# Kernel optimization log

Measured on AMD Instinct MI355X. Metric: run time of the kernel, lower is better.

## Reference

```python
import jax, jax.numpy as jnp
import numpy as np

N = 8192
D = 64  # node feature width
E = 64  # edge-derived feature width


def setup_inputs() -> dict:
    key = jax.random.key(0)
    k1, k2, k3 = jax.random.split(key, 3)
    # Dense normalized adjacency (module stores normalize(A).toarray()); values in [0,1).
    A = jax.random.uniform(k1, (N, N), dtype=jnp.float32) / N  # scaled like a normalized adjacency
    F = jax.random.normal(k2, (N, D), dtype=jnp.float32)
    new_features = jax.random.normal(k3, (N, E), dtype=jnp.float32)
    return {"A": A, "F": F, "new_features": new_features}


def reference(A, F, new_features):
    # layer 1: node branch gets ReLU, edge-feature branch does not
    h = jax.nn.relu(A @ F)              # [N, D]
    g = A @ new_features                # [N, E]
    # layer 2
    h = jax.nn.relu(A @ h)              # [N, D]
    g = A @ g                           # [N, E]
    return jnp.concatenate([h, g], axis=-1)  # [N, D+E]
```

## Files before the change

### kernel.cpp

```cpp
#include <hip/hip_runtime.h>
#include <hip/hip_bf16.h>


typedef unsigned short ushort_t;
typedef __attribute__((ext_vector_type(8))) short short8;
typedef __attribute__((ext_vector_type(4))) float f32x4;
typedef __attribute__((ext_vector_type(4))) unsigned short us4;

#define NN 8192
#define NO 128
#define BKK 64
#define KSPAN 2048
#define GITERS (KSPAN / BKK)

__global__ void detect_dtype(const ushort_t* __restrict__ A, int* __restrict__ flag) {
  __shared__ int smax, szero;
  const int t = threadIdx.x;
  if (t == 0) { smax = 0; szero = 0; }
  __syncthreads();
  int lmax = 0, lzero = 0;
  #pragma unroll
  for (int j = 0; j < 8; ++j) {
    int idx = t * 8 + j;
    int u = (int)A[idx];
    if ((idx & 1) == 0) {
      lmax = max(lmax, u);
      lzero += (u == 0) ? 1 : 0;
    }
  }
  atomicMax(&smax, lmax);
  atomicAdd(&szero, lzero);
  __syncthreads();
  if (t == 0) *flag = (smax > 0x3A00 || szero > 800) ? 1 : 0;
}

__global__ void zero_ws(float* __restrict__ p) {
  size_t i = ((size_t)blockIdx.x * 256 + threadIdx.x) * 4;
  *(float4*)(p + i) = make_float4(0.f, 0.f, 0.f, 0.f);
}

__device__ __forceinline__ short bf16bits(float x) {
  __hip_bfloat16 h = __float2bfloat16(x);
  return *reinterpret_cast<short*>(&h);
}

__device__ __forceinline__ short8 cvt8(float4 a, float4 b) {
  short8 r;
  r[0] = bf16bits(a.x); r[1] = bf16bits(a.y); r[2] = bf16bits(a.z); r[3] = bf16bits(a.w);
  r[4] = bf16bits(b.x); r[5] = bf16bits(b.y); r[6] = bf16bits(b.z); r[7] = bf16bits(b.w);
  return r;
}

__global__ void pack_bt(const ushort_t* __restrict__ F, const ushort_t* __restrict__ NF,
                        ushort_t* __restrict__ Bt, const int* __restrict__ flag) {
  int idx = blockIdx.x * 256 + threadIdx.x;
  int n = idx >> 10;
  int k0 = (idx & 1023) << 3;
  ushort_t* dst = Bt + ((size_t)n << 13) + k0;
  if (*flag) {
    const float* src = (n < 64) ? ((const float*)F + n) : ((const float*)NF + (n - 64));
    #pragma unroll
    for (int j = 0; j < 8; ++j) dst[j] = (ushort_t)bf16bits(src[(size_t)(k0 + j) << 6]);
  } else {
    const ushort_t* src = (n < 64) ? (F + n) : (NF + (n - 64));
    #pragma unroll
    for (int j = 0; j < 8; ++j) dst[j] = src[(size_t)(k0 + j) << 6];
  }
}

__device__ __forceinline__ void compute_tile(const ushort_t* bA, const ushort_t* bB,
                                             int w, int lane, f32x4 (&acc)[4][2]) {
  #pragma unroll
  for (int s = 0; s < 2; ++s) {
    short8 b0 = *(const short8*)(bB + (4 * w + s) * 512 + lane * 8);
    short8 b1 = *(const short8*)(bB + (4 * w + 2 + s) * 512 + lane * 8);
    #pragma unroll
    for (int mt = 0; mt < 4; ++mt) {
      short8 a = *(const short8*)(bA + (2 * mt + s) * 512 + lane * 8);
      acc[mt][0] = __builtin_amdgcn_mfma_f32_16x16x32_bf16(a, b0, acc[mt][0], 0, 0, 0);
      acc[mt][1] = __builtin_amdgcn_mfma_f32_16x16x32_bf16(a, b1, acc[mt][1], 0, 0, 0);
    }
  }
}

__global__ __launch_bounds__(256) void gemm_atomic(
    const ushort_t* __restrict__ Au, const float* __restrict__ Af,
    const ushort_t* __restrict__ Bt, float* __restrict__ P,
    const int* __restrict__ flag) {
  __shared__ __align__(16) ushort_t lsA[2][8 * 512];
  __shared__ __align__(16) ushort_t lsB[2][16 * 512];
  const int t = threadIdx.x;
  const int w = t >> 6, lane = t & 63;
  const int mtile = blockIdx.x >> 2;
  const int split = blockIdx.x & 3;
  const size_t m0 = (size_t)mtile * 64;
  const int kb = split * KSPAN;

  const int wh = w >> 1, ws_ = w & 1;
  const int l15 = lane & 15, lq = lane >> 4;
  const size_t rowA0 = m0 + (size_t)wh * 16 + l15;
  const size_t colb = (size_t)kb + ws_ * 32 + lq * 8;
  const ushort_t* gA0b = Au + rowA0 * NN + colb;
  const ushort_t* gA1b = gA0b + (size_t)32 * NN;
  const float*    gA0f = Af + rowA0 * NN + colb;
  const float*    gA1f = gA0f + (size_t)32 * NN;
  const ushort_t* gB0 = Bt + ((size_t)wh * 16 + l15) * NN + colb;

  const f32x4 zero = {0.f, 0.f, 0.f, 0.f};
  f32x4 acc[4][2];
  #pragma unroll
  for (int mt = 0; mt < 4; ++mt) { acc[mt][0] = zero; acc[mt][1] = zero; }

  const int fl = *flag;

  if (fl) {
    float4 a00 = *(const float4*)gA0f;
    float4 a01 = *(const float4*)(gA0f + 4);
    float4 a10 = *(const float4*)gA1f;
    float4 a11 = *(const float4*)(gA1f + 4);
    short8 rb0 = *(const short8*)gB0;
    short8 rb1 = *(const short8*)(gB0 + (size_t)32 * NN);
    short8 rb2 = *(const short8*)(gB0 + (size_t)64 * NN);
    short8 rb3 = *(const short8*)(gB0 + (size_t)96 * NN);
    gA0f += BKK; gA1f += BKK; gB0 += BKK;
    *(short8*)(lsA[0] + t * 8) = cvt8(a00, a01);
    *(short8*)(lsA[0] + t * 8 + 2048) = cvt8(a10, a11);
    *(short8*)(lsB[0] + t * 8) = rb0;
    *(short8*)(lsB[0] + t * 8 + 2048) = rb1;
    *(short8*)(lsB[0] + t * 8 + 4096) = rb2;
    *(short8*)(lsB[0] + t * 8 + 6144) = rb3;
    __syncthreads();
    int buf = 0;
    for (int it = 0; it < GITERS - 1; ++it) {
      a00 = *(const float4*)gA0f;
      a01 = *(const float4*)(gA0f + 4);
      a10 = *(const float4*)gA1f;
      a11 = *(const float4*)(gA1f + 4);
      rb0 = *(const short8*)gB0;
      rb1 = *(const short8*)(gB0 + (size_t)32 * NN);
      rb2 = *(const short8*)(gB0 + (size_t)64 * NN);
      rb3 = *(const short8*)(gB0 + (size_t)96 * NN);
      gA0f += BKK; gA1f += BKK; gB0 += BKK;
      compute_tile(lsA[buf], lsB[buf], w, lane, acc);
      const int nb = buf ^ 1;
      *(short8*)(lsA[nb] + t * 8) = cvt8(a00, a01);
      *(short8*)(lsA[nb] + t * 8 + 2048) = cvt8(a10, a11);
      *(short8*)(lsB[nb] + t * 8) = rb0;
      *(short8*)(lsB[nb] + t * 8 + 2048) = rb1;
      *(short8*)(lsB[nb] + t * 8 + 4096) = rb2;
      *(short8*)(lsB[nb] + t * 8 + 6144) = rb3;
      __syncthreads();
      buf = nb;
    }
    compute_tile(lsA[buf], lsB[buf], w, lane, acc);
  } else {
    short8 ra0 = *(const short8*)gA0b;
    short8 ra1 = *(const short8*)gA1b;
    short8 rb0 = *(const short8*)gB0;
    short8 rb1 = *(const short8*)(gB0 + (size_t)32 * NN);
    short8 rb2 = *(const short8*)(gB0 + (size_t)64 * NN);
    short8 rb3 = *(const short8*)(gB0 + (size_t)96 * NN);
    gA0b += BKK; gA1b += BKK; gB0 += BKK;
    *(short8*)(lsA[0] + t * 8) = ra0;
    *(short8*)(lsA[0] + t * 8 + 2048) = ra1;
    *(short8*)(lsB[0] + t * 8) = rb0;
    *(short8*)(lsB[0] + t * 8 + 2048) = rb1;
    *(short8*)(lsB[0] + t * 8 + 4096) = rb2;
    *(short8*)(lsB[0] + t * 8 + 6144) = rb3;
    __syncthreads();
    int buf = 0;
    for (int it = 0; it < GITERS - 1; ++it) {
      ra0 = *(const short8*)gA0b;
      ra1 = *(const short8*)gA1b;
      rb0 = *(const short8*)gB0;
      rb1 = *(const short8*)(gB0 + (size_t)32 * NN);
      rb2 = *(const short8*)(gB0 + (size_t)64 * NN);
      rb3 = *(const short8*)(gB0 + (size_t)96 * NN);
      gA0b += BKK; gA1b += BKK; gB0 += BKK;
      compute_tile(lsA[buf], lsB[buf], w, lane, acc);
      const int nb = buf ^ 1;
      *(short8*)(lsA[nb] + t * 8) = ra0;
      *(short8*)(lsA[nb] + t * 8 + 2048) = ra1;
      *(short8*)(lsB[nb] + t * 8) = rb0;
      *(short8*)(lsB[nb] + t * 8 + 2048) = rb1;
      *(short8*)(lsB[nb] + t * 8 + 4096) = rb2;
      *(short8*)(lsB[nb] + t * 8 + 6144) = rb3;
      __syncthreads();
      buf = nb;
    }
    compute_tile(lsA[buf], lsB[buf], w, lane, acc);
  }

  const int cn0 = 32 * w + l15;
  const int rb = lq * 4;
  #pragma unroll
  for (int mt = 0; mt < 4; ++mt) {
    float* dst = P + (m0 + mt * 16 + rb) * NO;
    #pragma unroll
    for (int reg = 0; reg < 4; ++reg) {
      unsafeAtomicAdd(&dst[(size_t)reg * NO + cn0], acc[mt][0][reg]);
      unsafeAtomicAdd(&dst[(size_t)reg * NO + cn0 + 16], acc[mt][1][reg]);
    }
  }
}

__global__ void epi_t(const float* __restrict__ P, ushort_t* __restrict__ Ct) {
  __shared__ ushort_t lt[128 * 65];
  const size_t base = (size_t)blockIdx.x * (64 * NO);
  const int t = threadIdx.x;
  for (int i = 0; i < 32; ++i) {
    int e = i * 256 + t;
    int n = e & 127, m = e >> 7;
    float v = P[base + e];
    if (n < 64) v = fmaxf(v, 0.f);
    lt[n * 65 + m] = (ushort_t)bf16bits(v);
  }
  __syncthreads();
  const int n = t >> 1, h = t & 1;
  const size_t m0 = (size_t)blockIdx.x * 64;
  ushort_t* dst = Ct + (size_t)n * NN + m0 + h * 32;
  #pragma unroll
  for (int j = 0; j < 32; ++j) dst[j] = lt[n * 65 + h * 32 + j];
}

__global__ void epi_out(const float* __restrict__ P, ushort_t* __restrict__ outb,
                        float* __restrict__ outf, const int* __restrict__ flag) {
  int idx = blockIdx.x * 256 + threadIdx.x;
  size_t e = (size_t)idx * 4;
  float4 v = *(const float4*)(P + e);
  float s[4] = {v.x, v.y, v.z, v.w};
  int n0 = (int)(e & 127);
  #pragma unroll
  for (int j = 0; j < 4; ++j) if (n0 + j < 64) s[j] = fmaxf(s[j], 0.f);
  if (*flag) {
    *(float4*)(outf + e) = make_float4(s[0], s[1], s[2], s[3]);
  } else {
    us4 r;
    #pragma unroll
    for (int j = 0; j < 4; ++j) r[j] = (ushort_t)bf16bits(s[j]);
    *(us4*)(outb + e) = r;
  }
}

extern "C" void kernel_launch(void* const* d_in, const int* in_sizes, int n_in,
                              void* d_out, int out_size, void* d_ws, size_t ws_size,
                              hipStream_t stream) {
  const ushort_t* A  = (const ushort_t*)d_in[0];
  const ushort_t* F  = (const ushort_t*)d_in[1];
  const ushort_t* NF = (const ushort_t*)d_in[2];

  char* ws = (char*)d_ws;
  ushort_t* Bt = (ushort_t*)(ws);
  ushort_t* Ct = (ushort_t*)(ws + (2u << 20));
  float*    P1 = (float*)(ws + (4u << 20));
  float*    P2 = (float*)(ws + (8u << 20));
  int*    flag = (int*)(ws + (12u << 20));

  detect_dtype<<<1, 256, 0, stream>>>(A, flag);
  zero_ws<<<2048, 256, 0, stream>>>(P1);
  pack_bt<<<512, 256, 0, stream>>>(F, NF, Bt, flag);
  gemm_atomic<<<512, 256, 0, stream>>>(A, (const float*)A, Bt, P1, flag);
  epi_t<<<128, 256, 0, stream>>>(P1, Ct);
  gemm_atomic<<<512, 256, 0, stream>>>(A, (const float*)A, Ct, P2, flag);
  epi_out<<<1024, 256, 0, stream>>>(P2, (ushort_t*)d_out, (float*)d_out, flag);
}
```

Before: 483.7 us.

## Cache bf16 copy of A in first GEMM, use direct global-to-LDS loads, split K by eight

On the fp32 input path, the first GEMM converts A to bf16 and also writes that copy to workspace, so the second GEMM can read half the bytes using global_load_lds direct copies. Split-K grows from 4 to 8, doubling the grid, and double buffering is replaced by single-buffered LDS with two barriers per iteration. The epi_t store loop is vectorised to 16-byte writes. This adds a 128MB workspace write in the first GEMM and drops prefetch overlap in exchange for reduced traffic in the second GEMM.

```diff
diff --git a/kernel.cpp b/kernel.cpp
--- a/kernel.cpp
+++ b/kernel.cpp
@@ -10,7 +10,8 @@
 #define NN 8192
 #define NO 128
 #define BKK 64
-#define KSPAN 2048
+#define NSPLIT 8
+#define KSPAN (NN / NSPLIT)
 #define GITERS (KSPAN / BKK)
 
 __global__ void detect_dtype(const ushort_t* __restrict__ A, int* __restrict__ flag) {
@@ -49,6 +50,12 @@
   r[0] = bf16bits(a.x); r[1] = bf16bits(a.y); r[2] = bf16bits(a.z); r[3] = bf16bits(a.w);
   r[4] = bf16bits(b.x); r[5] = bf16bits(b.y); r[6] = bf16bits(b.z); r[7] = bf16bits(b.w);
   return r;
+}
+
+__device__ __forceinline__ void gl2lds16(const ushort_t* g, ushort_t* l) {
+  __builtin_amdgcn_global_load_lds(
+      (const __attribute__((address_space(1))) void*)g,
+      (__attribute__((address_space(3))) void*)l, 16, 0, 0);
 }
 
 __global__ void pack_bt(const ushort_t* __restrict__ F, const ushort_t* __restrict__ NF,
@@ -85,14 +92,14 @@
 
 __global__ __launch_bounds__(256) void gemm_atomic(
     const ushort_t* __restrict__ Au, const float* __restrict__ Af,
-    const ushort_t* __restrict__ Bt, float* __restrict__ P,
-    const int* __restrict__ flag) {
-  __shared__ __align__(16) ushort_t lsA[2][8 * 512];
-  __shared__ __align__(16) ushort_t lsB[2][16 * 512];
+    ushort_t* __restrict__ Abf, const ushort_t* __restrict__ Bt,
+    float* __restrict__ P, const int* __restrict__ flag, int wb, int rdabf) {
+  __shared__ __align__(16) ushort_t lsA[8 * 512];
+  __shared__ __align__(16) ushort_t lsB[16 * 512];
   const int t = threadIdx.x;
   const int w = t >> 6, lane = t & 63;
-  const int mtile = blockIdx.x >> 2;
-  const int split = blockIdx.x & 3;
+  const int mtile = blockIdx.x >> 3;
+  const int split = blockIdx.x & 7;
   const size_t m0 = (size_t)mtile * 64;
   const int kb = split * KSPAN;
 
@@ -100,10 +107,8 @@
   const int l15 = lane & 15, lq = lane >> 4;
   const size_t rowA0 = m0 + (size_t)wh * 16 + l15;
   const size_t colb = (size_t)kb + ws_ * 32 + lq * 8;
-  const ushort_t* gA0b = Au + rowA0 * NN + colb;
-  const ushort_t* gA1b = gA0b + (size_t)32 * NN;
-  const float*    gA0f = Af + rowA0 * NN + colb;
-  const float*    gA1f = gA0f + (size_t)32 * NN;
+  const size_t offA0 = rowA0 * NN + colb;
+  const size_t offA1 = offA0 + (size_t)32 * NN;
   const ushort_t* gB0 = Bt + ((size_t)wh * 16 + l15) * NN + colb;
 
   const f32x4 zero = {0.f, 0.f, 0.f, 0.f};
@@ -113,82 +118,56 @@
 
   const int fl = *flag;
 
-  if (fl) {
-    float4 a00 = *(const float4*)gA0f;
-    float4 a01 = *(const float4*)(gA0f + 4);
-    float4 a10 = *(const float4*)gA1f;
-    float4 a11 = *(const float4*)(gA1f + 4);
-    short8 rb0 = *(const short8*)gB0;
-    short8 rb1 = *(const short8*)(gB0 + (size_t)32 * NN);
-    short8 rb2 = *(const short8*)(gB0 + (size_t)64 * NN);
-    short8 rb3 = *(const short8*)(gB0 + (size_t)96 * NN);
-    gA0f += BKK; gA1f += BKK; gB0 += BKK;
-    *(short8*)(lsA[0] + t * 8) = cvt8(a00, a01);
-    *(short8*)(lsA[0] + t * 8 + 2048) = cvt8(a10, a11);
-    *(short8*)(lsB[0] + t * 8) = rb0;
-    *(short8*)(lsB[0] + t * 8 + 2048) = rb1;
-    *(short8*)(lsB[0] + t * 8 + 4096) = rb2;
-    *(short8*)(lsB[0] + t * 8 + 6144) = rb3;
-    __syncthreads();
-    int buf = 0;
-    for (int it = 0; it < GITERS - 1; ++it) {
-      a00 = *(const float4*)gA0f;
-      a01 = *(const float4*)(gA0f + 4);
-      a10 = *(const float4*)gA1f;
-      a11 = *(const float4*)(gA1f + 4);
-      rb0 = *(const short8*)gB0;
-      rb1 = *(const short8*)(gB0 + (size_t)32 * NN);
-      rb2 = *(const short8*)(gB0 + (size_t)64 * NN);
-      rb3 = *(const short8*)(gB0 + (size_t)96 * NN);
+  if (fl && !rdabf) {
+    const float* gA0f = Af + offA0;
+    const float* gA1f = Af + offA1;
+    ushort_t* pW0 = Abf + offA0;
+    ushort_t* pW1 = Abf + offA1;
+    for (int it = 0; it < GITERS; ++it) {
+      float4 a00 = *(const float4*)gA0f;
+      float4 a01 = *(const float4*)(gA0f + 4);
+      float4 a10 = *(const float4*)gA1f;
+      float4 a11 = *(const float4*)(gA1f + 4);
+      short8 rb0 = *(const short8*)gB0;
+      short8 rb1 = *(const short8*)(gB0 + (size_t)32 * NN);
+      short8 rb2 = *(const short8*)(gB0 + (size_t)64 * NN);
+      short8 rb3 = *(const short8*)(gB0 + (size_t)96 * NN);
       gA0f += BKK; gA1f += BKK; gB0 += BKK;
-      compute_tile(lsA[buf], lsB[buf], w, lane, acc);
-      const int nb = buf ^ 1;
-      *(short8*)(lsA[nb] + t * 8) = cvt8(a00, a01);
-      *(short8*)(lsA[nb] + t * 8 + 2048) = cvt8(a10, a11);
-      *(short8*)(lsB[nb] + t * 8) = rb0;
-      *(short8*)(lsB[nb] + t * 8 + 2048) = rb1;
-      *(short8*)(lsB[nb] + t * 8 + 4096) = rb2;
-      *(short8*)(lsB[nb] + t * 8 + 6144) = rb3;
-      __syncthreads();
-      buf = nb;
-    }
-    compute_tile(lsA[buf], lsB[buf], w, lane, acc);
+      short8 c0 = cvt8(a00, a01);
+      short8 c1 = cvt8(a10, a11);
+      if (wb) {
+        *(short8*)pW0 = c0;
+        *(short8*)pW1 = c1;
+        pW0 += BKK; pW1 += BKK;
+      }
+      *(short8*)(lsA + t * 8) = c0;
+      *(short8*)(lsA + t * 8 + 2048) = c1;
+      *(short8*)(lsB + t * 8) = rb0;
+      *(short8*)(lsB + t * 8 + 2048) = rb1;
+      *(short8*)(lsB + t * 8 + 4096) = rb2;
+      *(short8*)(lsB + t * 8 + 6144) = rb3;
+      __syncthreads();
+      compute_tile(lsA, lsB, w, lane, acc);
+      __syncthreads();
+    }
   } else {
-    short8 ra0 = *(const short8*)gA0b;
-    short8 ra1 = *(const short8*)gA1b;
-    short8 rb0 = *(const short8*)gB0;
-    short8 rb1 = *(const short8*)(gB0 + (size_t)32 * NN);
-    short8 rb2 = *(const short8*)(gB0 + (size_t)64 * NN);
-    short8 rb3 = *(const short8*)(gB0 + (size_t)96 * NN);
-    gA0b += BKK; gA1b += BKK; gB0 += BKK;
-    *(short8*)(lsA[0] + t * 8) = ra0;
-    *(short8*)(lsA[0] + t * 8 + 2048) = ra1;
-    *(short8*)(lsB[0] + t * 8) = rb0;
-    *(short8*)(lsB[0] + t * 8 + 2048) = rb1;
-    *(short8*)(lsB[0] + t * 8 + 4096) = rb2;
-    *(short8*)(lsB[0] + t * 8 + 6144) = rb3;
-    __syncthreads();
-    int buf = 0;
-    for (int it = 0; it < GITERS - 1; ++it) {
-      ra0 = *(const short8*)gA0b;
-      ra1 = *(const short8*)gA1b;
-      rb0 = *(const short8*)gB0;
-      rb1 = *(const short8*)(gB0 + (size_t)32 * NN);
-      rb2 = *(const short8*)(gB0 + (size_t)64 * NN);
-      rb3 = *(const short8*)(gB0 + (size_t)96 * NN);
-      gA0b += BKK; gA1b += BKK; gB0 += BKK;
-      compute_tile(lsA[buf], lsB[buf], w, lane, acc);
-      const int nb = buf ^ 1;
-      *(short8*)(lsA[nb] + t * 8) = ra0;
-      *(short8*)(lsA[nb] + t * 8 + 2048) = ra1;
-      *(short8*)(lsB[nb] + t * 8) = rb0;
-      *(short8*)(lsB[nb] + t * 8 + 2048) = rb1;
-      *(short8*)(lsB[nb] + t * 8 + 4096) = rb2;
-      *(short8*)(lsB[nb] + t * 8 + 6144) = rb3;
-      __syncthreads();
-      buf = nb;
-    }
-    compute_tile(lsA[buf], lsB[buf], w, lane, acc);
+    const ushort_t* Ab = rdabf ? (const ushort_t*)Abf : Au;
+    const ushort_t* gA0 = Ab + offA0;
+    const ushort_t* gA1 = Ab + offA1;
+    ushort_t* dA0 = lsA + w * 512;
+    ushort_t* dA1 = lsA + w * 512 + 2048;
+    ushort_t* dB  = lsB + w * 512;
+    for (int it = 0; it < GITERS; ++it) {
+      gl2lds16(gA0, dA0);
+      gl2lds16(gA1, dA1);
+      #pragma unroll
+      for (int j = 0; j < 4; ++j)
+        gl2lds16(gB0 + (size_t)(32 * j) * NN, dB + j * 2048);
+      gA0 += BKK; gA1 += BKK; gB0 += BKK;
+      __syncthreads();
+      compute_tile(lsA, lsB, w, lane, acc);
+      __syncthreads();
+    }
   }
 
   const int cn0 = 32 * w + l15;
@@ -220,7 +199,12 @@
   const size_t m0 = (size_t)blockIdx.x * 64;
   ushort_t* dst = Ct + (size_t)n * NN + m0 + h * 32;
   #pragma unroll
-  for (int j = 0; j < 32; ++j) dst[j] = lt[n * 65 + h * 32 + j];
+  for (int jj = 0; jj < 4; ++jj) {
+    short8 v;
+    #pragma unroll
+    for (int j = 0; j < 8; ++j) v[j] = (short)lt[n * 65 + h * 32 + jj * 8 + j];
+    *(short8*)(dst + jj * 8) = v;
+  }
 }
 
 __global__ void epi_out(const float* __restrict__ P, ushort_t* __restrict__ outb,
@@ -255,12 +239,17 @@
   float*    P1 = (float*)(ws + (4u << 20));
   float*    P2 = (float*)(ws + (8u << 20));
   int*    flag = (int*)(ws + (12u << 20));
+  ushort_t* Abf = (ushort_t*)(ws + (16u << 20));
+
+  const int wsok = (ws_size >= ((size_t)144 << 20)) ? 1 : 0;
 
   detect_dtype<<<1, 256, 0, stream>>>(A, flag);
   zero_ws<<<2048, 256, 0, stream>>>(P1);
   pack_bt<<<512, 256, 0, stream>>>(F, NF, Bt, flag);
-  gemm_atomic<<<512, 256, 0, stream>>>(A, (const float*)A, Bt, P1, flag);
+  gemm_atomic<<<1024, 256, 0, stream>>>(A, (const float*)A, Abf, Bt, P1, flag,
+                                        wsok, 0);
   epi_t<<<128, 256, 0, stream>>>(P1, Ct);
-  gemm_atomic<<<512, 256, 0, stream>>>(A, (const float*)A, Ct, P2, flag);
+  gemm_atomic<<<1024, 256, 0, stream>>>(A, (const float*)A, Abf, Ct, P2, flag,
+                                        0, wsok);
   epi_out<<<1024, 256, 0, stream>>>(P2, (ushort_t*)d_out, (float*)d_out, flag);
 }
```

After: 493.2 us. Within noise of the previous version (+2.0%).
